# Kernel tuning notes

Measured on AMD Instinct MI355X. Metric: run time of the kernel, lower is better.

Reference implementation:

```python
import jax, jax.numpy as jnp
import numpy as np

B, N, F, G = 2, 8, 32, 32
EPS = 1e-8
elu = jax.nn.elu

def pconv(x, w, b):
    # pointwise Conv3d (1x1x1): x (..., C, D, H, W), w (O, C), b (O,)
    return jnp.einsum('...cdhw,oc->...odhw', x, w) + b[:, None, None, None]

def mean_var(x, weight):
    # weighted mean/variance over the num_images axis (axis=1), keepdims
    mean = jnp.sum(x * weight, axis=1, keepdims=True)
    var = jnp.sum(weight * (x - mean) ** 2, axis=1, keepdims=True)
    return mean, var

def setup_inputs() -> dict:
    key = jax.random.key(0)
    ks = jax.random.split(key, 20)
    def wmat(k, o, i):
        return jax.random.normal(k, (o, i), jnp.float32) * (1.0 / np.sqrt(i))
    return {
        'features': jax.random.normal(ks[0], (B, N, F, G, G, G), jnp.float32),
        'mask': jax.random.uniform(ks[1], (B, N, 1, G, G, G), jnp.float32),
        'voxel_depth': jax.random.normal(ks[2], (B, N, 1, G, G, G), jnp.float32),
        'voxel_dir': jax.random.normal(ks[3], (B, N, 3, G, G, G), jnp.float32),
        'rde_w1': wmat(ks[4], F // 2, 4), 'rde_b1': jnp.zeros((F // 2,), jnp.float32),
        'rde_w2': wmat(ks[5], F, F // 2), 'rde_b2': jnp.zeros((F,), jnp.float32),
        'base_w1': wmat(ks[6], 2 * F, 3 * F), 'base_b1': jnp.zeros((2 * F,), jnp.float32),
        'base_w2': wmat(ks[7], F, 2 * F), 'base_b2': jnp.zeros((F,), jnp.float32),
        'vis_w1': wmat(ks[8], F, F), 'vis_b1': jnp.zeros((F,), jnp.float32),
        'vis_w2': wmat(ks[9], F + 1, F), 'vis_b2': jnp.zeros((F + 1,), jnp.float32),
        'vis2_w1': wmat(ks[10], F, F), 'vis2_b1': jnp.zeros((F,), jnp.float32),
        'vis2_w2': wmat(ks[11], 1, F), 'vis2_b2': jnp.zeros((1,), jnp.float32),
        'stat_w': wmat(ks[12], F, 2 * F + 1), 'stat_b': jnp.zeros((F,), jnp.float32),
    }

def reference(features, mask, voxel_depth, voxel_dir,
              rde_w1, rde_b1, rde_w2, rde_b2,
              base_w1, base_b1, base_w2, base_b2,
              vis_w1, vis_b1, vis_w2, vis_b2,
              vis2_w1, vis2_b1, vis2_w2, vis2_b2,
              stat_w, stat_b):
    b, n = features.shape[:2]
    # ray/depth encoder (pointwise MLP over 4 channels)
    rde = jnp.concatenate([voxel_dir, voxel_depth], axis=2)  # (B,N,4,G,G,G)
    rde = elu(pconv(elu(pconv(rde, rde_w1, rde_b1)), rde_w2, rde_b2))
    feats = features + rde
    # mask-normalized weights over views
    weight = mask / (jnp.sum(mask, axis=1, keepdims=True) + EPS)
    mean, var = mean_var(feats, weight)
    gf = jnp.concatenate([mean, var], axis=2)  # (B,1,2F,G,G,G)
    x = jnp.concatenate([jnp.broadcast_to(gf, (b, n) + gf.shape[2:]), feats], axis=2)  # (B,N,3F,...)
    x = elu(pconv(elu(pconv(x, base_w1, base_b1)), base_w2, base_b2))
    xv = elu(pconv(elu(pconv(x * weight, vis_w1, vis_b1)), vis_w2, vis_b2))
    x_res, vis = xv[:, :, :-1], xv[:, :, -1:]
    vis = jax.nn.sigmoid(vis) * mask
    x = x + x_res
    vis = jax.nn.sigmoid(pconv(elu(pconv(x * vis, vis2_w1, vis2_b1)), vis2_w2, vis2_b2)) * mask
    weight = vis / (jnp.sum(vis, axis=1, keepdims=True) + EPS)
    mean, var = mean_var(x, weight)
    gf = jnp.concatenate([mean[:, 0], var[:, 0], jnp.mean(weight, axis=1)], axis=1)  # (B,2F+1,G,G,G)
    return elu(pconv(gf, stat_w, stat_b))  # (B,F,G,G,G)
```

## Files before the change

kernel.cpp:

```cpp
#include <hip/hip_runtime.h>


#define G3 32768
#define KP 72

typedef _Float16 h8 __attribute__((ext_vector_type(8)));
typedef _Float16 h4 __attribute__((ext_vector_type(4)));
typedef _Float16 h2 __attribute__((ext_vector_type(2)));
typedef float f4 __attribute__((ext_vector_type(4)));
typedef float f2 __attribute__((ext_vector_type(2)));
typedef float f4a __attribute__((ext_vector_type(4), aligned(4)));

#define WB() __builtin_amdgcn_wave_barrier()

__device__ __forceinline__ float eluf(float x) {
    return x > 0.0f ? x : __expf(x) - 1.0f;
}
__device__ __forceinline__ float sigmoidf(float x) {
    return 1.0f / (1.0f + __expf(-x));
}
__device__ __forceinline__ float red8v(float v) {
    v += __shfl_xor(v, 8, 64);
    v += __shfl_xor(v, 16, 64);
    v += __shfl_xor(v, 32, 64);
    return v;
}

#define WS_BW1G 0
#define WS_BW1F 4096
#define WS_BW2 6144
#define WS_VW1 8192
#define WS_VW2 9216
#define WS_V2W1 10752

__global__ void prep_kernel(const float* __restrict__ bw1,
                            const float* __restrict__ bw2,
                            const float* __restrict__ vw1,
                            const float* __restrict__ vw2,
                            const float* __restrict__ v2w1,
                            _Float16* __restrict__ wh) {
    int t = blockIdx.x * blockDim.x + threadIdx.x;
    int stride = gridDim.x * blockDim.x;
    for (int i = t; i < 4096; i += stride) {
        int o = i >> 6, k = i & 63;
        wh[WS_BW1G + i] = (_Float16)bw1[o * 96 + k];
    }
    for (int i = t; i < 2048; i += stride) {
        int o = i >> 5, k = i & 31;
        wh[WS_BW1F + i] = (_Float16)bw1[o * 96 + 64 + k];
    }
    for (int i = t; i < 2048; i += stride) wh[WS_BW2 + i] = (_Float16)bw2[i];
    for (int i = t; i < 1024; i += stride) wh[WS_VW1 + i] = (_Float16)vw1[i];
    for (int i = t; i < 1536; i += stride)
        wh[WS_VW2 + i] = (i < 1056) ? (_Float16)vw2[i] : (_Float16)0.0f;
    for (int i = t; i < 1024; i += stride) wh[WS_V2W1 + i] = (_Float16)v2w1[i];
}

template <int K, int KS, int MT>
__device__ __forceinline__ void mfma_pass(const _Float16* __restrict__ Wf,
                                          const _Float16* __restrict__ Y,
                                          int srck0, int pass, int lane,
                                          f4 acc[2][4]) {
    const int q = lane >> 4, nlo = lane & 15;
    h8 bf[2][KS];
#pragma unroll
    for (int j = 0; j < 2; ++j) {
        const _Float16* yc =
            Y + ((pass * 2 + j) * 16 + nlo) * KP + srck0 + q * 8;
#pragma unroll
        for (int kt = 0; kt < KS; ++kt) bf[j][kt] = *(const h8*)(yc + kt * 32);
    }
#pragma unroll
    for (int mt = 0; mt < MT; ++mt) {
        h8 af[KS];
#pragma unroll
        for (int kt = 0; kt < KS; ++kt)
            af[kt] = *(const h8*)(Wf + (mt * 16 + nlo) * K + q * 8 + kt * 32);
#pragma unroll
        for (int j = 0; j < 2; ++j)
#pragma unroll
            for (int kt = 0; kt < KS; ++kt)
                acc[j][mt] = __builtin_amdgcn_mfma_f32_16x16x32_f16(
                    af[kt], bf[j][kt], acc[j][mt], 0, 0, 0);
    }
}

template <int MT>
__device__ __forceinline__ void epi_pass(f4 acc[2][4],
                                         const float* __restrict__ bias,
                                         _Float16* __restrict__ Y, int dstk0,
                                         int pass, int lane) {
    const int q = lane >> 4, nlo = lane & 15;
#pragma unroll
    for (int j = 0; j < 2; ++j) {
        const int col = (pass * 2 + j) * 16 + nlo;
#pragma unroll
        for (int mt = 0; mt < MT; ++mt) {
            f4 bb = *(const f4*)(bias + mt * 16 + q * 4);
            h4 hv;
#pragma unroll
            for (int r = 0; r < 4; ++r)
                hv[r] = (_Float16)eluf(acc[j][mt][r] + bb[r]);
            *(h4*)(Y + col * KP + dstk0 + mt * 16 + q * 4) = hv;
        }
    }
}

__global__ __launch_bounds__(64, 2) void ibr_mfma(
    const float* __restrict__ features, const float* __restrict__ mask,
    const float* __restrict__ vdepth, const float* __restrict__ vdir,
    const float* __restrict__ rde_w1, const float* __restrict__ rde_b1,
    const float* __restrict__ rde_w2, const float* __restrict__ rde_b2,
    const float* __restrict__ base_b1, const float* __restrict__ base_b2,
    const float* __restrict__ vis_b1, const float* __restrict__ vis_b2,
    const float* __restrict__ vis2_b1, const float* __restrict__ vis2_w2,
    const float* __restrict__ vis2_b2, const float* __restrict__ stat_w,
    const float* __restrict__ stat_b, const _Float16* __restrict__ wh,
    float* __restrict__ out) {
    __shared__ _Float16 Y[64 * KP];

    const int lane = threadIdx.x;
    const int n = lane >> 3, vi = lane & 7;
    const int blk = blockIdx.x;
    const int b = blk >> 12;
    const int i = blk & 4095;
    const int v0 = (((i & 7) << 9) | (i >> 3)) << 3;
    const int bn = b * 8 + n;
    const int v = v0 + vi;

    const float m = mask[bn * G3 + v];
    const float r0 = vdir[(bn * 3 + 0) * G3 + v];
    const float r1 = vdir[(bn * 3 + 1) * G3 + v];
    const float r2 = vdir[(bn * 3 + 2) * G3 + v];
    const float r3 = vdepth[bn * G3 + v];
    float f[32];
#pragma unroll
    for (int c = 0; c < 32; ++c) f[c] = features[(bn * 32 + c) * G3 + v];

    float h16[16];
#pragma unroll
    for (int o = 0; o < 16; ++o) {
        float a = rde_b1[o] + rde_w1[o * 4 + 0] * r0 + rde_w1[o * 4 + 1] * r1 +
                  rde_w1[o * 4 + 2] * r2 + rde_w1[o * 4 + 3] * r3;
        h16[o] = eluf(a);
    }
#pragma unroll
    for (int o = 0; o < 32; ++o) {
        float a = rde_b2[o];
#pragma unroll
        for (int c = 0; c < 16; ++c) a += rde_w2[o * 16 + c] * h16[c];
        f[o] += eluf(a);
    }

    const float msum = red8v(m);
    const float invA = 1.0f / (msum + 1e-8f);
    const float wt = m * invA;
    const float sA = msum * invA;

    {
        _Float16* yl = Y + lane * KP;
#pragma unroll
        for (int g = 0; g < 4; ++g) {
            h8 t;
#pragma unroll
            for (int e = 0; e < 8; ++e) t[e] = (_Float16)f[g * 8 + e];
            *(h8*)(yl + g * 8) = t;
        }
    }
    WB();

    {
        const int pv = lane >> 3, u = lane & 7;
        const float kA = 2.0f - __shfl(sA, pv, 64);
        float wv_[8];
#pragma unroll
        for (int nn = 0; nn < 8; ++nn) wv_[nn] = __shfl(wt, nn * 8 + pv, 64);
#pragma unroll
        for (int t2 = 0; t2 < 2; ++t2) {
            const int dw = u + 8 * t2;
            float s0 = 0.f, s1 = 0.f, q0 = 0.f, q1 = 0.f;
#pragma unroll
            for (int nn = 0; nn < 8; ++nn) {
                const int col = nn * 8 + pv;
                h2 xv = *(const h2*)(Y + col * KP + dw * 2);
                const float wv = wv_[nn];
                const float x0 = (float)xv[0], x1 = (float)xv[1];
                s0 += wv * x0; q0 += wv * x0 * x0;
                s1 += wv * x1; q1 += wv * x1 * x1;
            }
            h2 hm = {(_Float16)s0, (_Float16)s1};
            h2 hv = {(_Float16)(q0 - s0 * s0 * kA),
                     (_Float16)(q1 - s1 * s1 * kA)};
            _Float16* g =
                Y + (pv * 8 + (dw >> 2)) * KP + 64 + ((2 * dw) & 7);
            *(h2*)g = hm;
            *(h2*)(g + 4 * KP) = hv;
        }
    }
    WB();

    {
        const int q = lane >> 4, nlo = lane & 15, vox = nlo & 7;
        f4 accgf[4] = {};
        {
            h8 bg0 = *(const h8*)(Y + (vox * 8 + q) * KP + 64);
            h8 bg1 = *(const h8*)(Y + (vox * 8 + 4 + q) * KP + 64);
#pragma unroll
            for (int mt = 0; mt < 4; ++mt) {
                h8 a0 =
                    *(const h8*)(wh + WS_BW1G + (mt * 16 + nlo) * 64 + q * 8);
                h8 a1 = *(const h8*)(wh + WS_BW1G + (mt * 16 + nlo) * 64 +
                                     q * 8 + 32);
                accgf[mt] = __builtin_amdgcn_mfma_f32_16x16x32_f16(
                    a0, bg0, accgf[mt], 0, 0, 0);
                accgf[mt] = __builtin_amdgcn_mfma_f32_16x16x32_f16(
                    a1, bg1, accgf[mt], 0, 0, 0);
            }
        }
#pragma unroll
        for (int pass = 0; pass < 2; ++pass) {
            f4 acc[2][4] = {};
            mfma_pass<32, 1, 4>(wh + WS_BW1F, Y, 0, pass, lane, acc);
#pragma unroll
            for (int j = 0; j < 2; ++j) {
                const int col = (pass * 2 + j) * 16 + nlo;
#pragma unroll
                for (int mt = 0; mt < 4; ++mt) {
                    f4 bb = *(const f4*)(base_b1 + mt * 16 + q * 4);
                    h4 hv;
#pragma unroll
                    for (int r = 0; r < 4; ++r)
                        hv[r] =
                            (_Float16)eluf(acc[j][mt][r] + accgf[mt][r] + bb[r]);
                    *(h4*)(Y + col * KP + mt * 16 + q * 4) = hv;
                }
            }
        }
    }
    WB();

#pragma unroll
    for (int pass = 0; pass < 2; ++pass) {
        f4 acc[2][4] = {};
        mfma_pass<64, 2, 2>(wh + WS_BW2, Y, 0, pass, lane, acc);
        const int q = lane >> 4, nlo = lane & 15;
#pragma unroll
        for (int j = 0; j < 2; ++j) {
            const int col = (pass * 2 + j) * 16 + nlo;
            const float w = __shfl(wt, col, 64);
#pragma unroll
            for (int mt = 0; mt < 2; ++mt) {
                f4 bb = *(const f4*)(base_b2 + mt * 16 + q * 4);
                h4 hx, hxw;
#pragma unroll
                for (int r = 0; r < 4; ++r) {
                    const float xv = eluf(acc[j][mt][r] + bb[r]);
                    hx[r] = (_Float16)xv;
                    hxw[r] = (_Float16)(xv * w);
                }
                *(h4*)(Y + col * KP + 32 + mt * 16 + q * 4) = hx;
                *(h4*)(Y + col * KP + mt * 16 + q * 4) = hxw;
            }
        }
    }
    WB();

#pragma unroll
    for (int pass = 0; pass < 2; ++pass) {
        f4 acc[2][4] = {};
        mfma_pass<32, 1, 2>(wh + WS_VW1, Y, 0, pass, lane, acc);
        epi_pass<2>(acc, vis_b1, Y, 0, pass, lane);
    }
    WB();

    float visn_s[4];
#pragma unroll
    for (int pass = 0; pass < 2; ++pass) {
        f4 acc[2][4] = {};
        mfma_pass<32, 1, 3>(wh + WS_VW2, Y, 0, pass, lane, acc);
        const int q = lane >> 4, nlo = lane & 15;
#pragma unroll
        for (int j = 0; j < 2; ++j) {
            const int col = (pass * 2 + j) * 16 + nlo;
#pragma unroll
            for (int mt = 0; mt < 2; ++mt) {
                f4 bb = *(const f4*)(vis_b2 + mt * 16 + q * 4);
                h4 hv;
#pragma unroll
                for (int r = 0; r < 4; ++r)
                    hv[r] = (_Float16)eluf(acc[j][mt][r] + bb[r]);
                *(h4*)(Y + col * KP + mt * 16 + q * 4) = hv;
            }
            {
                const float mcol = __shfl(m, col, 64);
                const float vv = acc[j][2][0] + vis_b2[32];
                visn_s[pass * 2 + j] = sigmoidf(eluf(vv)) * mcol;
            }
        }
    }
    WB();

    {
        const int pv = lane >> 3, u = lane & 7;
#pragma unroll
        for (int nn = 0; nn < 8; ++nn) {
            const int col = nn * 8 + pv;
            const float vn = __shfl(visn_s[nn >> 1], (nn & 1) * 8 + pv, 64);
#pragma unroll
            for (int t2 = 0; t2 < 2; ++t2) {
                const int dw = u + 8 * t2;
                h2 xr = *(const h2*)(Y + col * KP + dw * 2);
                h2 xo = *(const h2*)(Y + col * KP + 32 + dw * 2);
                const float x0 = (float)xo[0] + (float)xr[0];
                const float x1 = (float)xo[1] + (float)xr[1];
                h2 hx = {(_Float16)x0, (_Float16)x1};
                h2 hxv = {(_Float16)(x0 * vn), (_Float16)(x1 * vn)};
                *(h2*)(Y + col * KP + 32 + dw * 2) = hx;
                *(h2*)(Y + col * KP + dw * 2) = hxv;
            }
        }
    }
    WB();

#pragma unroll
    for (int pass = 0; pass < 2; ++pass) {
        f4 acc[2][4] = {};
        mfma_pass<32, 1, 2>(wh + WS_V2W1, Y, 0, pass, lane, acc);
        epi_pass<2>(acc, vis2_b1, Y, 0, pass, lane);
    }
    WB();

    float sCl, wt2;
    {
        const _Float16* yc = Y + lane * KP;
        float a0 = vis2_b2[0], a1 = 0.f;
#pragma unroll
        for (int t = 0; t < 16; ++t) {
            h2 p = *(const h2*)(yc + t * 2);
            if (t & 1)
                a1 += vis2_w2[t * 2] * (float)p[0] +
                      vis2_w2[t * 2 + 1] * (float)p[1];
            else
                a0 += vis2_w2[t * 2] * (float)p[0] +
                      vis2_w2[t * 2 + 1] * (float)p[1];
        }
        const float visv = sigmoidf(a0 + a1) * m;
        const float b0 = red8v(visv);
        const float invC = 1.0f / (b0 + 1e-8f);
        wt2 = visv * invC;
        sCl = b0 * invC;
    }
    WB();

    {
        const int pv = lane >> 3, u = lane & 7;
        const float kC = 2.0f - __shfl(sCl, pv, 64);
        float w2_[8];
#pragma unroll
        for (int nn = 0; nn < 8; ++nn) w2_[nn] = __shfl(wt2, nn * 8 + pv, 64);
#pragma unroll
        for (int t2 = 0; t2 < 2; ++t2) {
            const int dw = u + 8 * t2;
            float s0 = 0.f, s1 = 0.f, q0 = 0.f, q1 = 0.f;
#pragma unroll
            for (int nn = 0; nn < 8; ++nn) {
                const int col = nn * 8 + pv;
                h2 xv = *(const h2*)(Y + col * KP + 32 + dw * 2);
                const float wv = w2_[nn];
                const float x0 = (float)xv[0], x1 = (float)xv[1];
                s0 += wv * x0; q0 += wv * x0 * x0;
                s1 += wv * x1; q1 += wv * x1 * x1;
            }
            f2 mp = {s0, s1};
            f2 vp = {q0 - s0 * s0 * kC, q1 - s1 * s1 * kC};
            *(f2*)((float*)(Y + (4 * pv + t2) * KP) + 2 * u) = mp;
            *(f2*)((float*)(Y + (4 * pv + 2 + t2) * KP) + 2 * u) = vp;
        }
    }
    WB();

    {
        const int o = lane >> 1;
        const int vi0 = (lane & 1) * 4;
        const float wm_own = sCl * 0.125f;
        const float* row = stat_w + o * 65;
        float wmv[4];
#pragma unroll
        for (int k2 = 0; k2 < 4; ++k2) wmv[k2] = __shfl(wm_own, vi0 + k2, 64);
        float pr[4];
#pragma unroll
        for (int k2 = 0; k2 < 4; ++k2) pr[k2] = stat_b[o];
#pragma unroll
        for (int c4 = 0; c4 < 8; ++c4) {
            f4a wr = *(const f4a*)(row + c4 * 4);
            f4a ur = *(const f4a*)(row + 32 + c4 * 4);
#pragma unroll
            for (int k2 = 0; k2 < 4; ++k2) {
                const float* sm =
                    (const float*)(Y + (4 * (vi0 + k2) + (c4 >> 2)) * KP) +
                    (c4 & 3) * 4;
                const float* sv =
                    (const float*)(Y + (4 * (vi0 + k2) + 2 + (c4 >> 2)) * KP) +
                    (c4 & 3) * 4;
                f4 a = *(const f4*)sm;
                f4 bvv = *(const f4*)sv;
                pr[k2] += wr[0] * a[0] + wr[1] * a[1] + wr[2] * a[2] +
                          wr[3] * a[3] + ur[0] * bvv[0] + ur[1] * bvv[1] +
                          ur[2] * bvv[2] + ur[3] * bvv[3];
            }
        }
        const float wl = row[64];
        f4 res;
#pragma unroll
        for (int k2 = 0; k2 < 4; ++k2)
            res[k2] = eluf(pr[k2] + wl * wmv[k2]);
        *(f4*)(out + ((b * 32 + o) << 15) + v0 + vi0) = res;
    }
}

extern "C" void kernel_launch(void* const* d_in, const int* in_sizes, int n_in,
                              void* d_out, int out_size, void* d_ws,
                              size_t ws_size, hipStream_t stream) {
    const float* features = (const float*)d_in[0];
    const float* mask = (const float*)d_in[1];
    const float* vdepth = (const float*)d_in[2];
    const float* vdir = (const float*)d_in[3];
    const float* rde_w1 = (const float*)d_in[4];
    const float* rde_b1 = (const float*)d_in[5];
    const float* rde_w2 = (const float*)d_in[6];
    const float* rde_b2 = (const float*)d_in[7];
    const float* base_w1 = (const float*)d_in[8];
    const float* base_b1 = (const float*)d_in[9];
    const float* base_w2 = (const float*)d_in[10];
    const float* base_b2 = (const float*)d_in[11];
    const float* vis_w1 = (const float*)d_in[12];
    const float* vis_b1 = (const float*)d_in[13];
    const float* vis_w2 = (const float*)d_in[14];
    const float* vis_b2 = (const float*)d_in[15];
    const float* vis2_w1 = (const float*)d_in[16];
    const float* vis2_b1 = (const float*)d_in[17];
    const float* vis2_w2 = (const float*)d_in[18];
    const float* vis2_b2 = (const float*)d_in[19];
    const float* stat_w = (const float*)d_in[20];
    const float* stat_b = (const float*)d_in[21];

    _Float16* wh = (_Float16*)d_ws;
    prep_kernel<<<24, 256, 0, stream>>>(base_w1, base_w2, vis_w1, vis_w2,
                                        vis2_w1, wh);

    ibr_mfma<<<8192, 64, 0, stream>>>(
        features, mask, vdepth, vdir, rde_w1, rde_b1, rde_w2, rde_b2, base_b1,
        base_b2, vis_b1, vis_b2, vis2_b1, vis2_w2, vis2_b2, stat_w, stat_b, wh,
        (float*)d_out);
}
```

Measured before the change: 197.9 us.

## Split each voxel block across two waves with LDS sync between stages

The per-block work moves from one wavefront to two: each wave loads half the feature channels, computes half the ray encoder, and handles one of the two MFMA column passes per layer. The wave barriers become __syncthreads, and the per-view visibility values now go through a small LDS array instead of register shuffles. The aim is to halve per-wave serial latency and register pressure, which should allow more waves in flight per CU. The cost is block-level barriers between every stage, and the duplicated ray-encoder first layer and mask reductions now run in both waves.

```diff
diff --git a/kernel.cpp b/kernel.cpp
--- a/kernel.cpp
+++ b/kernel.cpp
@@ -10,8 +10,6 @@
 typedef float f4 __attribute__((ext_vector_type(4)));
 typedef float f2 __attribute__((ext_vector_type(2)));
 typedef float f4a __attribute__((ext_vector_type(4), aligned(4)));
-
-#define WB() __builtin_amdgcn_wave_barrier()
 
 __device__ __forceinline__ float eluf(float x) {
     return x > 0.0f ? x : __expf(x) - 1.0f;
@@ -106,7 +104,7 @@
     }
 }
 
-__global__ __launch_bounds__(64, 2) void ibr_mfma(
+__global__ __launch_bounds__(128, 6) void ibr_mfma(
     const float* __restrict__ features, const float* __restrict__ mask,
     const float* __restrict__ vdepth, const float* __restrict__ vdir,
     const float* __restrict__ rde_w1, const float* __restrict__ rde_b1,
@@ -118,8 +116,11 @@
     const float* __restrict__ stat_b, const _Float16* __restrict__ wh,
     float* __restrict__ out) {
     __shared__ _Float16 Y[64 * KP];
-
-    const int lane = threadIdx.x;
+    __shared__ float visn_lds[64];
+
+    const int tid = threadIdx.x;
+    const int w = tid >> 6;
+    const int lane = tid & 63;
     const int n = lane >> 3, vi = lane & 7;
     const int blk = blockIdx.x;
     const int b = blk >> 12;
@@ -133,9 +134,10 @@
     const float r1 = vdir[(bn * 3 + 1) * G3 + v];
     const float r2 = vdir[(bn * 3 + 2) * G3 + v];
     const float r3 = vdepth[bn * G3 + v];
-    float f[32];
-#pragma unroll
-    for (int c = 0; c < 32; ++c) f[c] = features[(bn * 32 + c) * G3 + v];
+    float f[16];
+#pragma unroll
+    for (int c = 0; c < 16; ++c)
+        f[c] = features[(bn * 32 + w * 16 + c) * G3 + v];
 
     float h16[16];
 #pragma unroll
@@ -145,10 +147,11 @@
         h16[o] = eluf(a);
     }
 #pragma unroll
-    for (int o = 0; o < 32; ++o) {
-        float a = rde_b2[o];
-#pragma unroll
-        for (int c = 0; c < 16; ++c) a += rde_w2[o * 16 + c] * h16[c];
+    for (int o = 0; o < 16; ++o) {
+        const int oo = w * 16 + o;
+        float a = rde_b2[oo];
+#pragma unroll
+        for (int c = 0; c < 16; ++c) a += rde_w2[oo * 16 + c] * h16[c];
         f[o] += eluf(a);
     }
 
@@ -158,46 +161,40 @@
     const float sA = msum * invA;
 
     {
-        _Float16* yl = Y + lane * KP;
-#pragma unroll
-        for (int g = 0; g < 4; ++g) {
+        _Float16* yl = Y + lane * KP + w * 16;
+#pragma unroll
+        for (int g = 0; g < 2; ++g) {
             h8 t;
 #pragma unroll
             for (int e = 0; e < 8; ++e) t[e] = (_Float16)f[g * 8 + e];
             *(h8*)(yl + g * 8) = t;
         }
     }
-    WB();
-
-    {
-        const int pv = lane >> 3, u = lane & 7;
+    __syncthreads();
+
+    {
+        const int pv = tid >> 4;
+        const int dw = tid & 15;
         const float kA = 2.0f - __shfl(sA, pv, 64);
         float wv_[8];
 #pragma unroll
         for (int nn = 0; nn < 8; ++nn) wv_[nn] = __shfl(wt, nn * 8 + pv, 64);
-#pragma unroll
-        for (int t2 = 0; t2 < 2; ++t2) {
-            const int dw = u + 8 * t2;
-            float s0 = 0.f, s1 = 0.f, q0 = 0.f, q1 = 0.f;
-#pragma unroll
-            for (int nn = 0; nn < 8; ++nn) {
-                const int col = nn * 8 + pv;
-                h2 xv = *(const h2*)(Y + col * KP + dw * 2);
-                const float wv = wv_[nn];
-                const float x0 = (float)xv[0], x1 = (float)xv[1];
-                s0 += wv * x0; q0 += wv * x0 * x0;
-                s1 += wv * x1; q1 += wv * x1 * x1;
-            }
-            h2 hm = {(_Float16)s0, (_Float16)s1};
-            h2 hv = {(_Float16)(q0 - s0 * s0 * kA),
-                     (_Float16)(q1 - s1 * s1 * kA)};
-            _Float16* g =
-                Y + (pv * 8 + (dw >> 2)) * KP + 64 + ((2 * dw) & 7);
-            *(h2*)g = hm;
-            *(h2*)(g + 4 * KP) = hv;
-        }
-    }
-    WB();
+        float s0 = 0.f, s1 = 0.f, q0 = 0.f, q1 = 0.f;
+#pragma unroll
+        for (int nn = 0; nn < 8; ++nn) {
+            h2 xv = *(const h2*)(Y + (nn * 8 + pv) * KP + dw * 2);
+            const float wv = wv_[nn];
+            const float x0 = (float)xv[0], x1 = (float)xv[1];
+            s0 += wv * x0; q0 += wv * x0 * x0;
+            s1 += wv * x1; q1 += wv * x1 * x1;
+        }
+        h2 hm = {(_Float16)s0, (_Float16)s1};
+        h2 hv = {(_Float16)(q0 - s0 * s0 * kA), (_Float16)(q1 - s1 * s1 * kA)};
+        _Float16* g = Y + (pv * 8 + (dw >> 2)) * KP + 64 + ((2 * dw) & 7);
+        *(h2*)g = hm;
+        *(h2*)(g + 4 * KP) = hv;
+    }
+    __syncthreads();
 
     {
         const int q = lane >> 4, nlo = lane & 15, vox = nlo & 7;
@@ -217,37 +214,32 @@
                     a1, bg1, accgf[mt], 0, 0, 0);
             }
         }
-#pragma unroll
-        for (int pass = 0; pass < 2; ++pass) {
-            f4 acc[2][4] = {};
-            mfma_pass<32, 1, 4>(wh + WS_BW1F, Y, 0, pass, lane, acc);
-#pragma unroll
-            for (int j = 0; j < 2; ++j) {
-                const int col = (pass * 2 + j) * 16 + nlo;
-#pragma unroll
-                for (int mt = 0; mt < 4; ++mt) {
-                    f4 bb = *(const f4*)(base_b1 + mt * 16 + q * 4);
-                    h4 hv;
-#pragma unroll
-                    for (int r = 0; r < 4; ++r)
-                        hv[r] =
-                            (_Float16)eluf(acc[j][mt][r] + accgf[mt][r] + bb[r]);
-                    *(h4*)(Y + col * KP + mt * 16 + q * 4) = hv;
-                }
-            }
-        }
-    }
-    WB();
-
-#pragma unroll
-    for (int pass = 0; pass < 2; ++pass) {
         f4 acc[2][4] = {};
-        mfma_pass<64, 2, 2>(wh + WS_BW2, Y, 0, pass, lane, acc);
+        mfma_pass<32, 1, 4>(wh + WS_BW1F, Y, 0, w, lane, acc);
+#pragma unroll
+        for (int j = 0; j < 2; ++j) {
+            const int col = (w * 2 + j) * 16 + nlo;
+#pragma unroll
+            for (int mt = 0; mt < 4; ++mt) {
+                f4 bb = *(const f4*)(base_b1 + mt * 16 + q * 4);
+                h4 hv;
+#pragma unroll
+                for (int r = 0; r < 4; ++r)
+                    hv[r] = (_Float16)eluf(acc[j][mt][r] + accgf[mt][r] + bb[r]);
+                *(h4*)(Y + col * KP + mt * 16 + q * 4) = hv;
+            }
+        }
+    }
+    __syncthreads();
+
+    {
+        f4 acc[2][4] = {};
+        mfma_pass<64, 2, 2>(wh + WS_BW2, Y, 0, w, lane, acc);
         const int q = lane >> 4, nlo = lane & 15;
 #pragma unroll
         for (int j = 0; j < 2; ++j) {
-            const int col = (pass * 2 + j) * 16 + nlo;
-            const float w = __shfl(wt, col, 64);
+            const int col = (w * 2 + j) * 16 + nlo;
+            const float wcol = __shfl(wt, col, 64);
 #pragma unroll
             for (int mt = 0; mt < 2; ++mt) {
                 f4 bb = *(const f4*)(base_b2 + mt * 16 + q * 4);
@@ -256,32 +248,29 @@
                 for (int r = 0; r < 4; ++r) {
                     const float xv = eluf(acc[j][mt][r] + bb[r]);
                     hx[r] = (_Float16)xv;
-                    hxw[r] = (_Float16)(xv * w);
+                    hxw[r] = (_Float16)(xv * wcol);
                 }
                 *(h4*)(Y + col * KP + 32 + mt * 16 + q * 4) = hx;
                 *(h4*)(Y + col * KP + mt * 16 + q * 4) = hxw;
             }
         }
     }
-    WB();
-
-#pragma unroll
-    for (int pass = 0; pass < 2; ++pass) {
+    __syncthreads();
+
+    {
         f4 acc[2][4] = {};
-        mfma_pass<32, 1, 2>(wh + WS_VW1, Y, 0, pass, lane, acc);
-        epi_pass<2>(acc, vis_b1, Y, 0, pass, lane);
-    }
-    WB();
-
-    float visn_s[4];
-#pragma unroll
-    for (int pass = 0; pass < 2; ++pass) {
+        mfma_pass<32, 1, 2>(wh + WS_VW1, Y, 0, w, lane, acc);
+        epi_pass<2>(acc, vis_b1, Y, 0, w, lane);
+    }
+    __syncthreads();
+
+    {
         f4 acc[2][4] = {};
-        mfma_pass<32, 1, 3>(wh + WS_VW2, Y, 0, pass, lane, acc);
+        mfma_pass<32, 1, 3>(wh + WS_VW2, Y, 0, w, lane, acc);
         const int q = lane >> 4, nlo = lane & 15;
 #pragma unroll
         for (int j = 0; j < 2; ++j) {
-            const int col = (pass * 2 + j) * 16 + nlo;
+            const int col = (w * 2 + j) * 16 + nlo;
 #pragma unroll
             for (int mt = 0; mt < 2; ++mt) {
                 f4 bb = *(const f4*)(vis_b2 + mt * 16 + q * 4);
@@ -291,44 +280,39 @@
                     hv[r] = (_Float16)eluf(acc[j][mt][r] + bb[r]);
                 *(h4*)(Y + col * KP + mt * 16 + q * 4) = hv;
             }
-            {
-                const float mcol = __shfl(m, col, 64);
+            const float mcol = __shfl(m, col, 64);
+            if (q == 0) {
                 const float vv = acc[j][2][0] + vis_b2[32];
-                visn_s[pass * 2 + j] = sigmoidf(eluf(vv)) * mcol;
-            }
-        }
-    }
-    WB();
-
-    {
-        const int pv = lane >> 3, u = lane & 7;
+                visn_lds[col] = sigmoidf(eluf(vv)) * mcol;
+            }
+        }
+    }
+    __syncthreads();
+
+    {
+        const int pv = tid >> 4, dw = tid & 15;
 #pragma unroll
         for (int nn = 0; nn < 8; ++nn) {
             const int col = nn * 8 + pv;
-            const float vn = __shfl(visn_s[nn >> 1], (nn & 1) * 8 + pv, 64);
-#pragma unroll
-            for (int t2 = 0; t2 < 2; ++t2) {
-                const int dw = u + 8 * t2;
-                h2 xr = *(const h2*)(Y + col * KP + dw * 2);
-                h2 xo = *(const h2*)(Y + col * KP + 32 + dw * 2);
-                const float x0 = (float)xo[0] + (float)xr[0];
-                const float x1 = (float)xo[1] + (float)xr[1];
-                h2 hx = {(_Float16)x0, (_Float16)x1};
-                h2 hxv = {(_Float16)(x0 * vn), (_Float16)(x1 * vn)};
-                *(h2*)(Y + col * KP + 32 + dw * 2) = hx;
-                *(h2*)(Y + col * KP + dw * 2) = hxv;
-            }
-        }
-    }
-    WB();
-
-#pragma unroll
-    for (int pass = 0; pass < 2; ++pass) {
+            const float vn = visn_lds[col];
+            h2 xr = *(const h2*)(Y + col * KP + dw * 2);
+            h2 xo = *(const h2*)(Y + col * KP + 32 + dw * 2);
+            const float x0 = (float)xo[0] + (float)xr[0];
+            const float x1 = (float)xo[1] + (float)xr[1];
+            h2 hx = {(_Float16)x0, (_Float16)x1};
+            h2 hxv = {(_Float16)(x0 * vn), (_Float16)(x1 * vn)};
+            *(h2*)(Y + col * KP + 32 + dw * 2) = hx;
+            *(h2*)(Y + col * KP + dw * 2) = hxv;
+        }
+    }
+    __syncthreads();
+
+    {
         f4 acc[2][4] = {};
-        mfma_pass<32, 1, 2>(wh + WS_V2W1, Y, 0, pass, lane, acc);
-        epi_pass<2>(acc, vis2_b1, Y, 0, pass, lane);
-    }
-    WB();
+        mfma_pass<32, 1, 2>(wh + WS_V2W1, Y, 0, w, lane, acc);
+        epi_pass<2>(acc, vis2_b1, Y, 0, w, lane);
+    }
+    __syncthreads();
 
     float sCl, wt2;
     {
@@ -350,52 +334,48 @@
         wt2 = visv * invC;
         sCl = b0 * invC;
     }
-    WB();
-
-    {
-        const int pv = lane >> 3, u = lane & 7;
+    __syncthreads();
+
+    {
+        const int pv = tid >> 4, dw = tid & 15;
         const float kC = 2.0f - __shfl(sCl, pv, 64);
         float w2_[8];
 #pragma unroll
         for (int nn = 0; nn < 8; ++nn) w2_[nn] = __shfl(wt2, nn * 8 + pv, 64);
-#pragma unroll
-        for (int t2 = 0; t2 < 2; ++t2) {
-            const int dw = u + 8 * t2;
-            float s0 = 0.f, s1 = 0.f, q0 = 0.f, q1 = 0.f;
-#pragma unroll
-            for (int nn = 0; nn < 8; ++nn) {
-                const int col = nn * 8 + pv;
-                h2 xv = *(const h2*)(Y + col * KP + 32 + dw * 2);
-                const float wv = w2_[nn];
-                const float x0 = (float)xv[0], x1 = (float)xv[1];
-                s0 += wv * x0; q0 += wv * x0 * x0;
-                s1 += wv * x1; q1 += wv * x1 * x1;
-            }
-            f2 mp = {s0, s1};
-            f2 vp = {q0 - s0 * s0 * kC, q1 - s1 * s1 * kC};
-            *(f2*)((float*)(Y + (4 * pv + t2) * KP) + 2 * u) = mp;
-            *(f2*)((float*)(Y + (4 * pv + 2 + t2) * KP) + 2 * u) = vp;
-        }
-    }
-    WB();
-
-    {
-        const int o = lane >> 1;
-        const int vi0 = (lane & 1) * 4;
+        float s0 = 0.f, s1 = 0.f, q0 = 0.f, q1 = 0.f;
+#pragma unroll
+        for (int nn = 0; nn < 8; ++nn) {
+            h2 xv = *(const h2*)(Y + (nn * 8 + pv) * KP + 32 + dw * 2);
+            const float wv = w2_[nn];
+            const float x0 = (float)xv[0], x1 = (float)xv[1];
+            s0 += wv * x0; q0 += wv * x0 * x0;
+            s1 += wv * x1; q1 += wv * x1 * x1;
+        }
+        f2 mp = {s0, s1};
+        f2 vp = {q0 - s0 * s0 * kC, q1 - s1 * s1 * kC};
+        const int t2 = dw >> 3, us = dw & 7;
+        *(f2*)((float*)(Y + (4 * pv + t2) * KP) + 2 * us) = mp;
+        *(f2*)((float*)(Y + (4 * pv + 2 + t2) * KP) + 2 * us) = vp;
+    }
+    __syncthreads();
+
+    {
+        const int o = tid >> 2;
+        const int vi0 = (tid & 3) * 2;
         const float wm_own = sCl * 0.125f;
         const float* row = stat_w + o * 65;
-        float wmv[4];
-#pragma unroll
-        for (int k2 = 0; k2 < 4; ++k2) wmv[k2] = __shfl(wm_own, vi0 + k2, 64);
-        float pr[4];
-#pragma unroll
-        for (int k2 = 0; k2 < 4; ++k2) pr[k2] = stat_b[o];
+        float wmv[2];
+#pragma unroll
+        for (int k2 = 0; k2 < 2; ++k2) wmv[k2] = __shfl(wm_own, vi0 + k2, 64);
+        float pr[2];
+#pragma unroll
+        for (int k2 = 0; k2 < 2; ++k2) pr[k2] = stat_b[o];
 #pragma unroll
         for (int c4 = 0; c4 < 8; ++c4) {
             f4a wr = *(const f4a*)(row + c4 * 4);
             f4a ur = *(const f4a*)(row + 32 + c4 * 4);
 #pragma unroll
-            for (int k2 = 0; k2 < 4; ++k2) {
+            for (int k2 = 0; k2 < 2; ++k2) {
                 const float* sm =
                     (const float*)(Y + (4 * (vi0 + k2) + (c4 >> 2)) * KP) +
                     (c4 & 3) * 4;
@@ -410,11 +390,8 @@
             }
         }
         const float wl = row[64];
-        f4 res;
-#pragma unroll
-        for (int k2 = 0; k2 < 4; ++k2)
-            res[k2] = eluf(pr[k2] + wl * wmv[k2]);
-        *(f4*)(out + ((b * 32 + o) << 15) + v0 + vi0) = res;
+        f2 res = {eluf(pr[0] + wl * wmv[0]), eluf(pr[1] + wl * wmv[1])};
+        *(f2*)(out + ((b * 32 + o) << 15) + v0 + vi0) = res;
     }
 }
 
@@ -448,7 +425,7 @@
     prep_kernel<<<24, 256, 0, stream>>>(base_w1, base_w2, vis_w1, vis_w2,
                                         vis2_w1, wh);
 
-    ibr_mfma<<<8192, 64, 0, stream>>>(
+    ibr_mfma<<<8192, 128, 0, stream>>>(
         features, mask, vdepth, vdir, rde_w1, rde_b1, rde_w2, rde_b2, base_b1,
         base_b2, vis_b1, vis_b2, vis2_b1, vis2_w2, vis2_b2, stat_w, stat_b, wh,
         (float*)d_out);
```

Result: slower. 271.6 us (+37.2%).
